# Kernel optimization log

Hardware: AMD Instinct MI355X
Metric: run time of the kernel (lower is better)

Reference implementation:

```python
import jax, jax.numpy as jnp
import numpy as np

N = 100000      # num nodes
E = 600000      # num edges
DIN = 64        # input_dim
DH = 128        # hidden_dim
G = 512         # num graphs
EPS = 1e-5      # BatchNorm eps


def setup_inputs() -> dict:
    key = jax.random.key(0)
    ks = jax.random.split(key, 12)
    x = jax.random.normal(ks[0], (N, DIN), jnp.float32)
    edge_index = jax.random.randint(ks[1], (2, E), 0, N)
    batch = jnp.sort(jax.random.randint(ks[2], (N,), 0, G))

    def w(k, shape):
        return (jax.random.normal(k, shape, jnp.float32) / np.float32(np.sqrt(shape[0])))

    inp = {"x": x, "edge_index": edge_index, "batch": batch}
    inp.update(
        W1=w(ks[3], (DIN, DH)), b1=jnp.zeros((DH,), jnp.float32),
        bn1_g=jnp.ones((DH,), jnp.float32), bn1_b=jnp.zeros((DH,), jnp.float32),
        bn1_m=jax.random.normal(ks[4], (DH,), jnp.float32) * 0.1,
        bn1_v=jnp.ones((DH,), jnp.float32),
        W2=w(ks[5], (DH, DH)), b2=jnp.zeros((DH,), jnp.float32),
        bn2_g=jnp.ones((DH,), jnp.float32), bn2_b=jnp.zeros((DH,), jnp.float32),
        bn2_m=jax.random.normal(ks[6], (DH,), jnp.float32) * 0.1,
        bn2_v=jnp.ones((DH,), jnp.float32),
        W3=w(ks[7], (DH, DH)), b3=jnp.zeros((DH,), jnp.float32),
        bn3_g=jnp.ones((DH,), jnp.float32), bn3_b=jnp.zeros((DH,), jnp.float32),
        bn3_m=jax.random.normal(ks[8], (DH,), jnp.float32) * 0.1,
        bn3_v=jnp.ones((DH,), jnp.float32),
        fc1_w=w(ks[9], (DH, DH // 2)), fc1_b=jnp.zeros((DH // 2,), jnp.float32),
        fc2_w=w(ks[10], (DH // 2, 1)), fc2_b=jnp.zeros((1,), jnp.float32),
    )
    return inp


def reference(x, edge_index, batch,
              W1, b1, bn1_g, bn1_b, bn1_m, bn1_v,
              W2, b2, bn2_g, bn2_b, bn2_m, bn2_v,
              W3, b3, bn3_g, bn3_b, bn3_m, bn3_v,
              fc1_w, fc1_b, fc2_w, fc2_b):
    # --- GCN normalization with self-loops (PyG GCNConv, sym norm) ---
    loop = jnp.arange(N, dtype=edge_index.dtype)
    src = jnp.concatenate([edge_index[0], loop])  # [E+N]
    dst = jnp.concatenate([edge_index[1], loop])  # [E+N]
    deg = jax.ops.segment_sum(jnp.ones_like(dst, jnp.float32), dst, num_segments=N)
    dis = jnp.where(deg > 0, jax.lax.rsqrt(jnp.maximum(deg, 1.0)), 0.0)
    norm = (dis[src] * dis[dst])[:, None]  # [E+N, 1]

    def conv(h, W, b):
        h = h @ W
        agg = jax.ops.segment_sum(h[src] * norm, dst, num_segments=N)
        return agg + b

    def bn(h, g, bta, m, v):
        return (h - m) * jax.lax.rsqrt(v + EPS) * g + bta  # eval-mode BatchNorm1d

    # block 1 (dropout is identity in eval)
    h = jax.nn.relu(bn(conv(x, W1, b1), bn1_g, bn1_b, bn1_m, bn1_v))
    # middle residual block (num_layers=3 -> one block)
    h = jax.nn.relu(bn(conv(h, W2, b2), bn2_g, bn2_b, bn2_m, bn2_v)) + h
    # output conv block
    h = jax.nn.relu(bn(conv(h, W3, b3), bn3_g, bn3_b, bn3_m, bn3_v))

    # global mean pool over graphs
    sums = jax.ops.segment_sum(h, batch, num_segments=G)          # [G, DH]
    cnt = jax.ops.segment_sum(jnp.ones((N, 1), h.dtype), batch, num_segments=G)
    pooled = sums / jnp.maximum(cnt, 1.0)

    h = jax.nn.relu(pooled @ fc1_w + fc1_b)
    return jax.nn.sigmoid(h @ fc2_w + fc2_b)  # [G, 1]
```

## Files before the change

### kernel.cpp

```cpp
#include <hip/hip_runtime.h>
#include <math.h>

#define N_NODES 100000
#define N_EDGES 600000
#define DIN     64
#define DH      128
#define NG      512
#define EPS_BN  1e-5f
#define SCAN_TPB 256
#define N_SCAN_BLK ((N_NODES + SCAN_TPB - 1) / SCAN_TPB)
#define G_EDGE   ((N_EDGES + 255) / 256)

typedef unsigned short u16;
typedef short s16x8 __attribute__((ext_vector_type(8)));
typedef float f32x4 __attribute__((ext_vector_type(4)));

__device__ __forceinline__ u16 f2bf(float x) {
    unsigned u = __builtin_bit_cast(unsigned, x);
    u += 0x7fffu + ((u >> 16) & 1u);
    return (u16)(u >> 16);
}
__device__ __forceinline__ float bf2f(u16 h) {
    unsigned u = ((unsigned)h) << 16;
    return __builtin_bit_cast(float, u);
}

#define PREP_WT1_BLKS  32
#define PREP_WT2_BLKS  64
#define PREP_WT3_BLKS  64
#define PREP_BN_BLKS   2
#define PREP_GB_BLKS   3
#define PREP_B0 G_EDGE
#define PREP_B1 (PREP_B0 + PREP_WT1_BLKS)
#define PREP_B2 (PREP_B1 + PREP_WT2_BLKS)
#define PREP_B3 (PREP_B2 + PREP_WT3_BLKS)
#define PREP_B4 (PREP_B3 + PREP_BN_BLKS)
#define PREP_TOTAL (PREP_B4 + PREP_GB_BLKS)

__device__ __forceinline__ void wt_body(const float* __restrict__ W, u16* __restrict__ Wt,
                                        int K, int idx) {
    if (idx >= K * DH) return;
    int k = idx / DH, n = idx % DH;
    Wt[(long)n * K + k] = f2bf(W[idx]);
}

__global__ __launch_bounds__(256) void degprep_kernel(
    const int* __restrict__ dst, int* __restrict__ deg,
    const float* __restrict__ W1, u16* __restrict__ Wt1,
    const float* __restrict__ W2, u16* __restrict__ Wt2,
    const float* __restrict__ W3, u16* __restrict__ Wt3,
    const float* b1, const float* g1, const float* bb1, const float* m1, const float* v1,
    const float* b2, const float* g2, const float* bb2, const float* m2, const float* v2,
    const float* b3, const float* g3, const float* bb3, const float* m3, const float* v3,
    float* __restrict__ sc, float* __restrict__ sh,
    const int* __restrict__ batch, int* __restrict__ gp) {
    const int b = blockIdx.x;
    const int tid = threadIdx.x;
    if (b < PREP_B0) {
        const int e = b * 256 + tid;
        if (e < N_EDGES) atomicAdd(&deg[dst[e]], 1);
    } else if (b < PREP_B1) {
        wt_body(W1, Wt1, DIN, (b - PREP_B0) * 256 + tid);
    } else if (b < PREP_B2) {
        wt_body(W2, Wt2, DH, (b - PREP_B1) * 256 + tid);
    } else if (b < PREP_B3) {
        wt_body(W3, Wt3, DH, (b - PREP_B2) * 256 + tid);
    } else if (b < PREP_B4) {
        const int i = (b - PREP_B3) * 256 + tid;
        if (i < 3 * DH) {
            int l = i >> 7, c = i & (DH - 1);
            const float* bc = l == 0 ? b1 : (l == 1 ? b2 : b3);
            const float* g  = l == 0 ? g1 : (l == 1 ? g2 : g3);
            const float* bb = l == 0 ? bb1 : (l == 1 ? bb2 : bb3);
            const float* m  = l == 0 ? m1 : (l == 1 ? m2 : m3);
            const float* v  = l == 0 ? v1 : (l == 1 ? v2 : v3);
            float s = g[c] * rsqrtf(v[c] + EPS_BN);
            sc[i] = s;
            sh[i] = (bc[c] - m[c]) * s + bb[c];
        }
    } else {
        const int g = (b - PREP_B4) * 256 + tid;
        if (g <= NG) {
            int lo = 0, hi = N_NODES;
            while (lo < hi) {
                int mid = (lo + hi) >> 1;
                if (batch[mid] < g) lo = mid + 1; else hi = mid;
            }
            gp[g] = lo;
        }
    }
}

__global__ __launch_bounds__(SCAN_TPB) void scan1_kernel(const int* __restrict__ deg,
                                                         float* __restrict__ dis,
                                                         int* __restrict__ rp,
                                                         int* __restrict__ blk, int n) {
    __shared__ int sm[SCAN_TPB];
    const int t = threadIdx.x;
    const int i = blockIdx.x * SCAN_TPB + t;
    int v = 0;
    if (i < n) {
        v = deg[i];
        dis[i] = rsqrtf((float)v + 1.0f);
    }
    sm[t] = v;
    __syncthreads();
#pragma unroll
    for (int off = 1; off < SCAN_TPB; off <<= 1) {
        int u = (t >= off) ? sm[t - off] : 0;
        __syncthreads();
        sm[t] += u;
        __syncthreads();
    }
    if (i <= n) rp[i] = sm[t] - v;
    if (t == SCAN_TPB - 1) blk[blockIdx.x] = sm[t];
}

__global__ __launch_bounds__(512) void scan2_kernel(int* __restrict__ blk, int nblk) {
    __shared__ int sm[512];
    const int t = threadIdx.x;
    const int v = (t < nblk) ? blk[t] : 0;
    sm[t] = v;
    __syncthreads();
#pragma unroll
    for (int off = 1; off < 512; off <<= 1) {
        int u = (t >= off) ? sm[t - off] : 0;
        __syncthreads();
        sm[t] += u;
        __syncthreads();
    }
    if (t < nblk) blk[t] = sm[t] - v;
}

#define CSRX_XCVT_BLKS 3125
#define CSRX_TOTAL (G_EDGE + CSRX_XCVT_BLKS)
__global__ __launch_bounds__(256) void csr_xcvt_kernel(const int* __restrict__ src,
                                                       const int* __restrict__ dst,
                                                       const int* __restrict__ rp,
                                                       const int* __restrict__ blk,
                                                       int* __restrict__ cursor,
                                                       int* __restrict__ col,
                                                       const float* __restrict__ x,
                                                       const float* __restrict__ dis,
                                                       u16* __restrict__ xb) {
    const int b = blockIdx.x;
    const int tid = threadIdx.x;
    if (b < G_EDGE) {
        const int e = b * 256 + tid;
        if (e >= N_EDGES) return;
        const int s = src[e];
        const int d = dst[e];
        const int p = atomicAdd(&cursor[d], 1);
        col[rp[d] + blk[d >> 8] + p] = s;
    } else {
        const long base = ((long)(b - G_EDGE) * 256 + tid) * 8;
        const float dd = dis[base >> 6];
        const float4 a = *(const float4*)(x + base);
        const float4 c = *(const float4*)(x + base + 4);
        s16x8 o;
        o[0] = (short)f2bf(a.x * dd); o[1] = (short)f2bf(a.y * dd);
        o[2] = (short)f2bf(a.z * dd); o[3] = (short)f2bf(a.w * dd);
        o[4] = (short)f2bf(c.x * dd); o[5] = (short)f2bf(c.y * dd);
        o[6] = (short)f2bf(c.z * dd); o[7] = (short)f2bf(c.w * dd);
        *(s16x8*)(xb + base) = o;
    }
}

__global__ __launch_bounds__(256) void agg64_kernel(const u16* __restrict__ xb,
                                                    const int* __restrict__ rp,
                                                    const int* __restrict__ blk,
                                                    const int* __restrict__ col,
                                                    const float* __restrict__ dis,
                                                    u16* __restrict__ aggX, int n) {
    const long t = (long)blockIdx.x * blockDim.x + threadIdx.x;
    const int lane = (int)(t & 31);
    const long i = t >> 5;
    if (i >= n) return;
    const int cl = lane & 7;
    const int eh = (lane >> 3) & 3;
    const int c = cl * 8;

    float acc[8] = {0, 0, 0, 0, 0, 0, 0, 0};
    if (eh == 0) {
        const s16x8 hv = *(const s16x8*)(xb + i * DIN + c);
#pragma unroll
        for (int q = 0; q < 8; ++q) acc[q] = bf2f((u16)hv[q]);
    }

    const int beg = rp[i] + blk[i >> 8];
    const int end = rp[i + 1] + blk[(int)(i + 1) >> 8];
    for (int e = beg + eh; e < end; e += 4) {
        const int s = col[e];
        const s16x8 v = *(const s16x8*)(xb + (long)s * DIN + c);
#pragma unroll
        for (int q = 0; q < 8; ++q) acc[q] += bf2f((u16)v[q]);
    }

#pragma unroll
    for (int q = 0; q < 8; ++q) acc[q] += __shfl_xor(acc[q], 8);
#pragma unroll
    for (int q = 0; q < 8; ++q) acc[q] += __shfl_xor(acc[q], 16);

    if (eh == 0 && (lane >> 4) == 0) {
        const float dd = dis[i];
        s16x8 ov;
#pragma unroll
        for (int q = 0; q < 8; ++q) ov[q] = (short)f2bf(acc[q] * dd);
        *(s16x8*)(aggX + i * DIN + c) = ov;
    }
}

template <int K, bool BN_EPI>
__global__ __launch_bounds__(256) void gemm_mfma(const u16* __restrict__ A,
                                                 const u16* __restrict__ Wt,
                                                 const float* __restrict__ dis,
                                                 const float* __restrict__ scl,
                                                 const float* __restrict__ shf,
                                                 u16* __restrict__ C,
                                                 int M) {
    __shared__ u16 ldsc[4][16][DH];
    const int wave = threadIdx.x >> 6;
    const int lane = threadIdx.x & 63;
    const int r16 = lane & 15;
    const int kc  = lane >> 4;
    const long row0 = (long)blockIdx.x * 64 + wave * 16;

    f32x4 acc[8];
#pragma unroll
    for (int t = 0; t < 8; ++t)
#pragma unroll
        for (int q = 0; q < 4; ++q) acc[t][q] = 0.0f;

    long arow = row0 + r16;
    if (arow >= M) arow = M - 1;

#pragma unroll
    for (int ks = 0; ks < K; ks += 32) {
        const s16x8 a = *(const s16x8*)(A + arow * K + ks + kc * 8);
#pragma unroll
        for (int t = 0; t < 8; ++t) {
            const s16x8 b = *(const s16x8*)(Wt + (long)(t * 16 + r16) * K + ks + kc * 8);
            acc[t] = __builtin_amdgcn_mfma_f32_16x16x32_bf16(a, b, acc[t], 0, 0, 0);
        }
    }

    float dd[4], scv[8], shv[8];
    if constexpr (BN_EPI) {
#pragma unroll
        for (int t = 0; t < 8; ++t) {
            scv[t] = scl[t * 16 + r16];
            shv[t] = shf[t * 16 + r16];
        }
    } else {
#pragma unroll
        for (int q = 0; q < 4; ++q) {
            long r = row0 + kc * 4 + q;
            dd[q] = dis[r < M ? r : (M - 1)];
        }
    }

#pragma unroll
    for (int t = 0; t < 8; ++t) {
        const int blkc = (t << 1) | (r16 >> 3);
        const int co = r16 & 7;
#pragma unroll
        for (int q = 0; q < 4; ++q) {
            const int row = kc * 4 + q;
            float y;
            if constexpr (BN_EPI) {
                y = fmaxf(fmaf(acc[t][q], scv[t], shv[t]), 0.0f);
            } else {
                y = acc[t][q] * dd[q];
            }
            ldsc[wave][row][(((blkc ^ (row & 7)) << 3) | co)] = f2bf(y);
        }
    }
#pragma unroll
    for (int it = 0; it < 4; ++it) {
        const int rl = (lane >> 4) + it * 4;
        const long row = row0 + rl;
        if (row < M) {
            const int phys = (lane & 15) ^ (rl & 7);
            const s16x8 v = *(const s16x8*)&ldsc[wave][rl][phys << 3];
            *(s16x8*)(C + row * DH + ((lane & 15) << 3)) = v;
        }
    }
}

template <bool RES>
__global__ __launch_bounds__(256) void agg_epi_kernel(const u16* __restrict__ H,
                                                      const int* __restrict__ rp,
                                                      const int* __restrict__ blk,
                                                      const int* __restrict__ col,
                                                      const float* __restrict__ dis,
                                                      const float* __restrict__ scl,
                                                      const float* __restrict__ shf,
                                                      u16* __restrict__ out, int n) {
    const long t = (long)blockIdx.x * blockDim.x + threadIdx.x;
    const int lane = (int)(t & 31);
    const long i = t >> 5;
    if (i >= n) return;
    const int cl = lane & 15;
    const int eh = lane >> 4;
    const int c = cl * 8;

    float acc[8] = {0, 0, 0, 0, 0, 0, 0, 0};
    if (eh == 0) {
        const s16x8 hv = *(const s16x8*)(H + i * DH + c);
#pragma unroll
        for (int q = 0; q < 8; ++q) acc[q] = bf2f((u16)hv[q]);
    }

    const int beg = rp[i] + blk[i >> 8];
    const int end = rp[i + 1] + blk[(int)(i + 1) >> 8];
    for (int e = beg + eh; e < end; e += 2) {
        const int s = col[e];
        const s16x8 v = *(const s16x8*)(H + (long)s * DH + c);
#pragma unroll
        for (int q = 0; q < 8; ++q) acc[q] += bf2f((u16)v[q]);
    }

#pragma unroll
    for (int q = 0; q < 8; ++q) acc[q] += __shfl_xor(acc[q], 16);

    if (eh == 0) {
        const float dd = dis[i];
        const float4 s0 = *(const float4*)(scl + c);
        const float4 s1 = *(const float4*)(scl + c + 4);
        const float4 f0 = *(const float4*)(shf + c);
        const float4 f1 = *(const float4*)(shf + c + 4);
        const float sv[8] = {s0.x, s0.y, s0.z, s0.w, s1.x, s1.y, s1.z, s1.w};
        const float fv[8] = {f0.x, f0.y, f0.z, f0.w, f1.x, f1.y, f1.z, f1.w};

        float r[8];
#pragma unroll
        for (int q = 0; q < 8; ++q) r[q] = fmaxf(fmaf(acc[q] * dd, sv[q], fv[q]), 0.0f);
        if (RES) {
            const s16x8 rv = *(const s16x8*)(out + i * DH + c);
#pragma unroll
            for (int q = 0; q < 8; ++q) r[q] += bf2f((u16)rv[q]);
        }
        s16x8 ov;
#pragma unroll
        for (int q = 0; q < 8; ++q) ov[q] = (short)f2bf(r[q]);
        __builtin_nontemporal_store(ov, (s16x8*)(out + i * DH + c));
    }
}

__global__ __launch_bounds__(256) void pool_head_kernel(const u16* __restrict__ h,
                                                        const int* __restrict__ gp,
                                                        const float* __restrict__ fc1w,
                                                        const float* __restrict__ fc1b,
                                                        const float* __restrict__ fc2w,
                                                        const float* __restrict__ fc2b,
                                                        float* __restrict__ out) {
    const int g = blockIdx.x;
    const int t = threadIdx.x;
    const int grp = t >> 4;
    const int cl = t & 15;
    const int c = cl * 8;
    const int beg = gp[g];
    const int end = gp[g + 1];

    float acc[8] = {0, 0, 0, 0, 0, 0, 0, 0};
    for (int i = beg + grp; i < end; i += 16) {
        const s16x8 v = *(const s16x8*)(h + (long)i * DH + c);
#pragma unroll
        for (int q = 0; q < 8; ++q) acc[q] += bf2f((u16)v[q]);
    }

    __shared__ float sm[16][DH];
    __shared__ float p[DH];
#pragma unroll
    for (int q = 0; q < 8; ++q) sm[grp][c + q] = acc[q];
    __syncthreads();

    if (t < DH) {
        float s = 0.0f;
#pragma unroll
        for (int r = 0; r < 16; ++r) s += sm[r][t];
        p[t] = s / fmaxf((float)(end - beg), 1.0f);
    }
    __syncthreads();

    if (t < 64) {
        float a = 0.0f;
#pragma unroll 4
        for (int k = 0; k < DH; ++k) a = fmaf(p[k], fc1w[(long)k * 64 + t], a);
        const float h1 = fmaxf(a + fc1b[t], 0.0f);
        float v = h1 * fc2w[t];
#pragma unroll
        for (int off = 32; off > 0; off >>= 1) v += __shfl_down(v, off);
        if (t == 0) out[g] = 1.0f / (1.0f + expf(-(v + fc2b[0])));
    }
}

extern "C" void kernel_launch(void* const* d_in, const int* in_sizes, int n_in,
                              void* d_out, int out_size, void* d_ws, size_t ws_size,
                              hipStream_t stream) {
    const float* x     = (const float*)d_in[0];
    const int*   ei    = (const int*)d_in[1];
    const int*   batch = (const int*)d_in[2];
    const float* W1 = (const float*)d_in[3];
    const float* b1 = (const float*)d_in[4];
    const float* g1 = (const float*)d_in[5];
    const float* t1 = (const float*)d_in[6];
    const float* m1 = (const float*)d_in[7];
    const float* v1 = (const float*)d_in[8];
    const float* W2 = (const float*)d_in[9];
    const float* b2 = (const float*)d_in[10];
    const float* g2 = (const float*)d_in[11];
    const float* t2 = (const float*)d_in[12];
    const float* m2 = (const float*)d_in[13];
    const float* v2 = (const float*)d_in[14];
    const float* W3 = (const float*)d_in[15];
    const float* b3 = (const float*)d_in[16];
    const float* g3 = (const float*)d_in[17];
    const float* t3 = (const float*)d_in[18];
    const float* m3 = (const float*)d_in[19];
    const float* v3 = (const float*)d_in[20];
    const float* fc1w = (const float*)d_in[21];
    const float* fc1b = (const float*)d_in[22];
    const float* fc2w = (const float*)d_in[23];
    const float* fc2b = (const float*)d_in[24];

    const int* src = ei;
    const int* dst = ei + N_EDGES;

    char* ws = (char*)d_ws;
    size_t off = 0;
    auto alloc = [&](size_t bytes) -> char* {
        char* p = ws + off;
        off = (off + bytes + 511) & ~(size_t)511;
        return p;
    };
    int*   deg     = (int*)  alloc((size_t)2 * N_NODES * 4);
    int*   cursor  = deg + N_NODES;
    float* dis     = (float*)alloc((size_t)N_NODES * 4);
    int*   rp      = (int*)  alloc(((size_t)N_NODES + 1) * 4);
    int*   blk     = (int*)  alloc((size_t)N_SCAN_BLK * 4);
    int*   col     = (int*)  alloc((size_t)N_EDGES * 4);
    int*   gp      = (int*)  alloc((size_t)(NG + 1) * 4);
    float* bnsc    = (float*)alloc((size_t)3 * DH * 4);
    float* bnsh    = (float*)alloc((size_t)3 * DH * 4);
    u16*   Wt1     = (u16*)  alloc((size_t)DH * DIN * 2);
    u16*   Wt2     = (u16*)  alloc((size_t)DH * DH * 2);
    u16*   Wt3     = (u16*)  alloc((size_t)DH * DH * 2);
    u16*   xb      = (u16*)  alloc((size_t)N_NODES * DIN * 2);
    u16*   aggX    = (u16*)  alloc((size_t)N_NODES * DIN * 2);
    u16*   bufB    = (u16*)  alloc((size_t)N_NODES * DH * 2);
    u16*   bufA    = (u16*)  alloc((size_t)N_NODES * DH * 2);

    const int TPB = 256;
    const int gGemm = (N_NODES + 63) / 64;
    const int gAgg  = (int)(((long)N_NODES * 32 + TPB - 1) / TPB);

    hipMemsetAsync(deg, 0, (size_t)2 * N_NODES * 4, stream);
    degprep_kernel<<<PREP_TOTAL, TPB, 0, stream>>>(dst, deg, W1, Wt1, W2, Wt2, W3, Wt3,
                                                   b1, g1, t1, m1, v1,
                                                   b2, g2, t2, m2, v2,
                                                   b3, g3, t3, m3, v3,
                                                   bnsc, bnsh, batch, gp);
    scan1_kernel<<<N_SCAN_BLK, SCAN_TPB, 0, stream>>>(deg, dis, rp, blk, N_NODES);
    scan2_kernel<<<1, 512, 0, stream>>>(blk, N_SCAN_BLK);
    csr_xcvt_kernel<<<CSRX_TOTAL, TPB, 0, stream>>>(src, dst, rp, blk, cursor, col,
                                                    x, dis, xb);

    agg64_kernel<<<gAgg, TPB, 0, stream>>>(xb, rp, blk, col, dis, aggX, N_NODES);
    gemm_mfma<DIN, true><<<gGemm, TPB, 0, stream>>>(aggX, Wt1, dis, bnsc, bnsh, bufA,
                                                    N_NODES);
    gemm_mfma<DH, false><<<gGemm, TPB, 0, stream>>>(bufA, Wt2, dis, bnsc, bnsh, bufB,
                                                    N_NODES);
    agg_epi_kernel<true><<<gAgg, TPB, 0, stream>>>(bufB, rp, blk, col, dis,
                                                   bnsc + DH, bnsh + DH, bufA, N_NODES);
    gemm_mfma<DH, false><<<gGemm, TPB, 0, stream>>>(bufA, Wt3, dis, bnsc, bnsh, bufB,
                                                    N_NODES);
    agg_epi_kernel<false><<<gAgg, TPB, 0, stream>>>(bufB, rp, blk, col, dis,
                                                    bnsc + 2 * DH, bnsh + 2 * DH, bufA,
                                                    N_NODES);

    pool_head_kernel<<<NG, TPB, 0, stream>>>(bufA, gp, fc1w, fc1b, fc2w, fc2b,
                                             (float*)d_out);
}
```

Baseline: 280.6 us.

## Fuse layer-1 and layer-2 GEMMs and merge two-pass scan via last-block completion

```diff
diff --git a/kernel.cpp b/kernel.cpp
--- a/kernel.cpp
+++ b/kernel.cpp
@@ -91,11 +91,13 @@
     }
 }
 
-__global__ __launch_bounds__(SCAN_TPB) void scan1_kernel(const int* __restrict__ deg,
-                                                         float* __restrict__ dis,
-                                                         int* __restrict__ rp,
-                                                         int* __restrict__ blk, int n) {
+__global__ __launch_bounds__(SCAN_TPB) void scan_kernel(const int* __restrict__ deg,
+                                                        float* __restrict__ dis,
+                                                        int* __restrict__ rp,
+                                                        int* __restrict__ blk,
+                                                        int* __restrict__ done, int n) {
     __shared__ int sm[SCAN_TPB];
+    __shared__ int sflag;
     const int t = threadIdx.x;
     const int i = blockIdx.x * SCAN_TPB + t;
     int v = 0;
@@ -114,22 +116,35 @@
     }
     if (i <= n) rp[i] = sm[t] - v;
     if (t == SCAN_TPB - 1) blk[blockIdx.x] = sm[t];
-}
-
-__global__ __launch_bounds__(512) void scan2_kernel(int* __restrict__ blk, int nblk) {
-    __shared__ int sm[512];
-    const int t = threadIdx.x;
-    const int v = (t < nblk) ? blk[t] : 0;
-    sm[t] = v;
+
     __syncthreads();
-#pragma unroll
-    for (int off = 1; off < 512; off <<= 1) {
+    if (t == 0) {
+        __threadfence();
+        const int r = atomicAdd(done, 1);
+        sflag = (r == (int)gridDim.x - 1);
+    }
+    __syncthreads();
+    if (!sflag) return;
+
+    int a0 = (2 * t < N_SCAN_BLK)
+                 ? __hip_atomic_load(&blk[2 * t], __ATOMIC_RELAXED, __HIP_MEMORY_SCOPE_AGENT)
+                 : 0;
+    int a1 = (2 * t + 1 < N_SCAN_BLK)
+                 ? __hip_atomic_load(&blk[2 * t + 1], __ATOMIC_RELAXED, __HIP_MEMORY_SCOPE_AGENT)
+                 : 0;
+    const int s = a0 + a1;
+    sm[t] = s;
+    __syncthreads();
+#pragma unroll
+    for (int off = 1; off < SCAN_TPB; off <<= 1) {
         int u = (t >= off) ? sm[t - off] : 0;
         __syncthreads();
         sm[t] += u;
         __syncthreads();
     }
-    if (t < nblk) blk[t] = sm[t] - v;
+    const int ex = sm[t] - s;
+    if (2 * t < N_SCAN_BLK) blk[2 * t] = ex;
+    if (2 * t + 1 < N_SCAN_BLK) blk[2 * t + 1] = ex + a0;
 }
 
 #define CSRX_XCVT_BLKS 3125
@@ -210,12 +225,118 @@
     }
 }
 
-template <int K, bool BN_EPI>
+__global__ __launch_bounds__(256) void gemm12_kernel(const u16* __restrict__ aggX,
+                                                     const u16* __restrict__ Wt1,
+                                                     const u16* __restrict__ Wt2,
+                                                     const float* __restrict__ dis,
+                                                     const float* __restrict__ scl,
+                                                     const float* __restrict__ shf,
+                                                     u16* __restrict__ bufA,
+                                                     u16* __restrict__ bufB,
+                                                     int M) {
+    __shared__ u16 ldsc[4][16][DH];
+    const int wave = threadIdx.x >> 6;
+    const int lane = threadIdx.x & 63;
+    const int r16 = lane & 15;
+    const int kc  = lane >> 4;
+    const long row0 = (long)blockIdx.x * 64 + wave * 16;
+
+    long arow = row0 + r16;
+    if (arow >= M) arow = M - 1;
+
+    f32x4 acc[8];
+#pragma unroll
+    for (int t = 0; t < 8; ++t)
+#pragma unroll
+        for (int q = 0; q < 4; ++q) acc[t][q] = 0.0f;
+
+#pragma unroll
+    for (int ks = 0; ks < DIN; ks += 32) {
+        const s16x8 a = *(const s16x8*)(aggX + arow * DIN + ks + kc * 8);
+#pragma unroll
+        for (int t = 0; t < 8; ++t) {
+            const s16x8 b = *(const s16x8*)(Wt1 + (long)(t * 16 + r16) * DIN + ks + kc * 8);
+            acc[t] = __builtin_amdgcn_mfma_f32_16x16x32_bf16(a, b, acc[t], 0, 0, 0);
+        }
+    }
+
+    float scv[8], shv[8];
+#pragma unroll
+    for (int t = 0; t < 8; ++t) {
+        scv[t] = scl[t * 16 + r16];
+        shv[t] = shf[t * 16 + r16];
+    }
+
+#pragma unroll
+    for (int t = 0; t < 8; ++t) {
+        const int blkc = (t << 1) | (r16 >> 3);
+        const int co = r16 & 7;
+#pragma unroll
+        for (int q = 0; q < 4; ++q) {
+            const int row = kc * 4 + q;
+            const float y = fmaxf(fmaf(acc[t][q], scv[t], shv[t]), 0.0f);
+            ldsc[wave][row][(((blkc ^ (row & 7)) << 3) | co)] = f2bf(y);
+        }
+    }
+#pragma unroll
+    for (int it = 0; it < 4; ++it) {
+        const int rl = (lane >> 4) + it * 4;
+        const long row = row0 + rl;
+        if (row < M) {
+            const int phys = (lane & 15) ^ (rl & 7);
+            const s16x8 v = *(const s16x8*)&ldsc[wave][rl][phys << 3];
+            *(s16x8*)(bufA + row * DH + ((lane & 15) << 3)) = v;
+        }
+    }
+
+#pragma unroll
+    for (int t = 0; t < 8; ++t)
+#pragma unroll
+        for (int q = 0; q < 4; ++q) acc[t][q] = 0.0f;
+
+#pragma unroll
+    for (int ks = 0; ks < 4; ++ks) {
+        const int pb = (ks * 4 + kc) ^ (r16 & 7);
+        const s16x8 a = *(const s16x8*)&ldsc[wave][r16][pb << 3];
+#pragma unroll
+        for (int t = 0; t < 8; ++t) {
+            const s16x8 b = *(const s16x8*)(Wt2 + (long)(t * 16 + r16) * DH + ks * 32 + kc * 8);
+            acc[t] = __builtin_amdgcn_mfma_f32_16x16x32_bf16(a, b, acc[t], 0, 0, 0);
+        }
+    }
+
+    float dd[4];
+#pragma unroll
+    for (int q = 0; q < 4; ++q) {
+        long r = row0 + kc * 4 + q;
+        dd[q] = dis[r < M ? r : (M - 1)];
+    }
+
+#pragma unroll
+    for (int t = 0; t < 8; ++t) {
+        const int blkc = (t << 1) | (r16 >> 3);
+        const int co = r16 & 7;
+#pragma unroll
+        for (int q = 0; q < 4; ++q) {
+            const int row = kc * 4 + q;
+            ldsc[wave][row][(((blkc ^ (row & 7)) << 3) | co)] = f2bf(acc[t][q] * dd[q]);
+        }
+    }
+#pragma unroll
+    for (int it = 0; it < 4; ++it) {
+        const int rl = (lane >> 4) + it * 4;
+        const long row = row0 + rl;
+        if (row < M) {
+            const int phys = (lane & 15) ^ (rl & 7);
+            const s16x8 v = *(const s16x8*)&ldsc[wave][rl][phys << 3];
+            *(s16x8*)(bufB + row * DH + ((lane & 15) << 3)) = v;
+        }
+    }
+}
+
 __global__ __launch_bounds__(256) void gemm_mfma(const u16* __restrict__ A,
                                                  const u16* __restrict__ Wt,
                                                  const float* __restrict__ dis,
-                                                 const float* __restrict__ scl,
-                                                 const float* __restrict__ shf,
                                                  u16* __restrict__ C,
                                                  int M) {
     __shared__ u16 ldsc[4][16][DH];
@@ -235,28 +356,20 @@
     if (arow >= M) arow = M - 1;
 
 #pragma unroll
-    for (int ks = 0; ks < K; ks += 32) {
-        const s16x8 a = *(const s16x8*)(A + arow * K + ks + kc * 8);
+    for (int ks = 0; ks < DH; ks += 32) {
+        const s16x8 a = *(const s16x8*)(A + arow * DH + ks + kc * 8);
 #pragma unroll
         for (int t = 0; t < 8; ++t) {
-            const s16x8 b = *(const s16x8*)(Wt + (long)(t * 16 + r16) * K + ks + kc * 8);
+            const s16x8 b = *(const s16x8*)(Wt + (long)(t * 16 + r16) * DH + ks + kc * 8);
             acc[t] = __builtin_amdgcn_mfma_f32_16x16x32_bf16(a, b, acc[t], 0, 0, 0);
         }
     }
 
-    float dd[4], scv[8], shv[8];
-    if constexpr (BN_EPI) {
-#pragma unroll
-        for (int t = 0; t < 8; ++t) {
-            scv[t] = scl[t * 16 + r16];
-            shv[t] = shf[t * 16 + r16];
-        }
-    } else {
-#pragma unroll
-        for (int q = 0; q < 4; ++q) {
-            long r = row0 + kc * 4 + q;
-            dd[q] = dis[r < M ? r : (M - 1)];
-        }
+    float dd[4];
+#pragma unroll
+    for (int q = 0; q < 4; ++q) {
+        long r = row0 + kc * 4 + q;
+        dd[q] = dis[r < M ? r : (M - 1)];
     }
 
 #pragma unroll
@@ -266,13 +379,7 @@
 #pragma unroll
         for (int q = 0; q < 4; ++q) {
             const int row = kc * 4 + q;
-            float y;
-            if constexpr (BN_EPI) {
-                y = fmaxf(fmaf(acc[t][q], scv[t], shv[t]), 0.0f);
-            } else {
-                y = acc[t][q] * dd[q];
-            }
-            ldsc[wave][row][(((blkc ^ (row & 7)) << 3) | co)] = f2bf(y);
+            ldsc[wave][row][(((blkc ^ (row & 7)) << 3) | co)] = f2bf(acc[t][q] * dd[q]);
         }
     }
 #pragma unroll
@@ -434,8 +541,9 @@
         off = (off + bytes + 511) & ~(size_t)511;
         return p;
     };
-    int*   deg     = (int*)  alloc((size_t)2 * N_NODES * 4);
+    int*   deg     = (int*)  alloc(((size_t)2 * N_NODES + 256) * 4);
     int*   cursor  = deg + N_NODES;
+    int*   done    = deg + 2 * N_NODES;
     float* dis     = (float*)alloc((size_t)N_NODES * 4);
     int*   rp      = (int*)  alloc(((size_t)N_NODES + 1) * 4);
     int*   blk     = (int*)  alloc((size_t)N_SCAN_BLK * 4);
@@ -455,26 +563,22 @@
     const int gGemm = (N_NODES + 63) / 64;
     const int gAgg  = (int)(((long)N_NODES * 32 + TPB - 1) / TPB);
 
-    hipMemsetAsync(deg, 0, (size_t)2 * N_NODES * 4, stream);
+    hipMemsetAsync(deg, 0, ((size_t)2 * N_NODES + 256) * 4, stream);
     degprep_kernel<<<PREP_TOTAL, TPB, 0, stream>>>(dst, deg, W1, Wt1, W2, Wt2, W3, Wt3,
                                                    b1, g1, t1, m1, v1,
                                                    b2, g2, t2, m2, v2,
                                                    b3, g3, t3, m3, v3,
                                                    bnsc, bnsh, batch, gp);
-    scan1_kernel<<<N_SCAN_BLK, SCAN_TPB, 0, stream>>>(deg, dis, rp, blk, N_NODES);
-    scan2_kernel<<<1, 512, 0, stream>>>(blk, N_SCAN_BLK);
+    scan_kernel<<<N_SCAN_BLK, SCAN_TPB, 0, stream>>>(deg, dis, rp, blk, done, N_NODES);
     csr_xcvt_kernel<<<CSRX_TOTAL, TPB, 0, stream>>>(src, dst, rp, blk, cursor, col,
                                                     x, dis, xb);
 
     agg64_kernel<<<gAgg, TPB, 0, stream>>>(xb, rp, blk, col, dis, aggX, N_NODES);
-    gemm_mfma<DIN, true><<<gGemm, TPB, 0, stream>>>(aggX, Wt1, dis, bnsc, bnsh, bufA,
-                                                    N_NODES);
-    gemm_mfma<DH, false><<<gGemm, TPB, 0, stream>>>(bufA, Wt2, dis, bnsc, bnsh, bufB,
-                                                    N_NODES);
+    gemm12_kernel<<<gGemm, TPB, 0, stream>>>(aggX, Wt1, Wt2, dis, bnsc, bnsh,
+                                             bufA, bufB, N_NODES);
     agg_epi_kernel<true><<<gAgg, TPB, 0, stream>>>(bufB, rp, blk, col, dis,
                                                    bnsc + DH, bnsh + DH, bufA, N_NODES);
-    gemm_mfma<DH, false><<<gGemm, TPB, 0, stream>>>(bufA, Wt3, dis, bnsc, bnsh, bufB,
-                                                    N_NODES);
+    gemm_mfma<<<gGemm, TPB, 0, stream>>>(bufA, Wt3, dis, bufB, N_NODES);
     agg_epi_kernel<false><<<gAgg, TPB, 0, stream>>>(bufB, rp, blk, col, dis,
                                                     bnsc + 2 * DH, bnsh + 2 * DH, bufA,
                                                     N_NODES);
```

Result: slower. 287.3 us (median of 3 runs) (+2.4%).
